# Optimization experiments

Measured on AMD Instinct MI355X. Metric: run time of the kernel, lower is better.

Reference implementation:

```python
import jax, jax.numpy as jnp
import numpy as np

EPS = 1e-5

def _conv3x3(x, w, b):
    # x: [B,C,H,W], w: [O,I,3,3], b: [O]; padding=1 preserves HxW
    y = jax.lax.conv_general_dilated(
        x, w, window_strides=(1, 1), padding=((1, 1), (1, 1)),
        dimension_numbers=('NCHW', 'OIHW', 'NCHW'))
    return y + b[None, :, None, None]

def _instance_norm(x):
    # InstanceNorm2d(affine=False): normalize over spatial dims per (sample, channel)
    mu = jnp.mean(x, axis=(2, 3), keepdims=True)
    var = jnp.var(x, axis=(2, 3), keepdims=True)
    return (x - mu) * jax.lax.rsqrt(var + EPS)

def setup_inputs() -> dict:
    key = jax.random.key(0)
    k1, k2, k3 = jax.random.split(key, 3)
    B, Cin, Cout, H, W = 8, 32, 64, 320, 320
    x = jax.random.normal(k1, (B, Cin, H, W), dtype=jnp.float32)
    w1 = jax.random.normal(k2, (Cout, Cin, 3, 3), dtype=jnp.float32) * (1.0 / np.sqrt(Cin * 9))
    b1 = jnp.zeros((Cout,), dtype=jnp.float32)
    w2 = jax.random.normal(k3, (Cout, Cout, 3, 3), dtype=jnp.float32) * (1.0 / np.sqrt(Cout * 9))
    b2 = jnp.zeros((Cout,), dtype=jnp.float32)
    return {"x": x, "w1": w1, "b1": b1, "w2": w2, "b2": b2}

def reference(x, w1, b1, w2, b2):
    # conv1 -> InstanceNorm -> ReLU -> (Dropout p=0 identity)
    h = jax.nn.relu(_instance_norm(_conv3x3(x, w1, b1)))
    # conv2 -> InstanceNorm -> ReLU -> (Dropout p=0 identity)
    out = jax.nn.relu(_instance_norm(_conv3x3(h, w2, b2)))
    return out
```

## Files before the change

kernel.cpp:

```cpp
#include <hip/hip_runtime.h>

#define HH 320
#define WW 320
#define BB 8
static constexpr float EPS = 1e-5f;

typedef __attribute__((ext_vector_type(8))) short bf16x8;
typedef __attribute__((ext_vector_type(4))) float f32x4;

__device__ inline float bf2f(unsigned short u) {
    union { unsigned int i; float f; } v; v.i = ((unsigned int)u) << 16; return v.f;
}
__device__ inline unsigned short f2bf(float f) {
    union { float f; unsigned int i; } v; v.f = f;
    unsigned int r = v.i + 0x7fffu + ((v.i >> 16) & 1u);
    return (unsigned short)(r >> 16);
}
__device__ inline unsigned int cvtpk(float a, float b) {
    unsigned int r;
    asm volatile("v_cvt_pk_bf16_f32 %0, %1, %2" : "=v"(r) : "v"(a), "v"(b));
    return r;
}
__device__ inline void glds16(const void* g, void* l) {
    __builtin_amdgcn_global_load_lds(
        (const __attribute__((address_space(1))) unsigned int*)g,
        (__attribute__((address_space(3))) unsigned int*)l, 16, 0, 0);
}

__global__ __launch_bounds__(256) void prep_hwc(const float* __restrict__ in,
                                                unsigned short* __restrict__ out)
{
    __shared__ float sT[32][65];
    const int tid = threadIdx.x;
    const int x0  = blockIdx.x * 64;
    const int y   = blockIdx.y;
    const int b   = blockIdx.z;
    for (int e = tid; e < 32 * 64; e += 256) {
        int c = e >> 6, x = e & 63;
        sT[c][x] = in[(((size_t)(b * 32 + c) * HH) + y) * WW + x0 + x];
    }
    __syncthreads();
    for (int e = tid; e < 64 * 32; e += 256) {
        int x = e >> 5, c = e & 31;
        out[((((size_t)b * HH + y) * WW) + x0 + x) * 32 + c] = f2bf(sT[c][x]);
    }
}

__global__ __launch_bounds__(256) void wprep_swz(const float* __restrict__ w1,
                                                 const float* __restrict__ w2,
                                                 unsigned short* __restrict__ wt1,
                                                 unsigned short* __restrict__ wt2)
{
    int i = blockIdx.x * 256 + threadIdx.x;
    if (i < 2304) {
        int s = i & 3, oc = (i >> 2) & 63, kk = i >> 8;
        int icq = s ^ ((oc >> 1) & 3);
        const float* src = w1 + ((size_t)oc * 32 + icq * 8) * 9 + kk;
        unsigned short pk[8];
#pragma unroll
        for (int j = 0; j < 8; ++j) pk[j] = f2bf(src[j * 9]);
        *(bf16x8*)&wt1[(size_t)i * 8] = *(bf16x8*)pk;
    }
    if (i < 4608) {
        int icc = i / 2304, u = i - icc * 2304;
        int s = u & 3, oc = (u >> 2) & 63, kk = u >> 8;
        int icq = s ^ ((oc >> 1) & 3);
        const float* src = w2 + ((size_t)oc * 64 + icc * 32 + icq * 8) * 9 + kk;
        unsigned short pk[8];
#pragma unroll
        for (int j = 0; j < 8; ++j) pk[j] = f2bf(src[j * 9]);
        *(bf16x8*)&wt2[(size_t)i * 8] = *(bf16x8*)pk;
    }
}

__global__ __launch_bounds__(256) void wfold(const unsigned short* __restrict__ wt2,
                                             const float* __restrict__ b2,
                                             const float2* __restrict__ stats1,
                                             unsigned short* __restrict__ wt2b,
                                             float* __restrict__ bias2b)
{
    __shared__ float sMu[64], sR[64];
    __shared__ float sBias[256];
    const int b = blockIdx.x, tid = threadIdx.x;
    if (tid < 64) {
        float2 ms = stats1[b * 64 + tid];
        sMu[tid] = bf2f(f2bf(ms.x));
        sR[tid]  = ms.y;
    }
    __syncthreads();
    const int oc = tid & 63, rep = tid >> 6;
    float bsum = 0.f;
    for (int cs = rep * 2; cs < rep * 2 + 2; ++cs) {
        int icc = cs >> 2, s = cs & 3;
        int icq = s ^ ((oc >> 1) & 3);
        for (int kk = 0; kk < 9; ++kk) {
            size_t u = (size_t)icc * 2304 + kk * 256 + oc * 4 + s;
            bf16x8 v = *(const bf16x8*)&wt2[u * 8];
            unsigned short o8[8];
#pragma unroll
            for (int j = 0; j < 8; ++j) {
                int ic = icc * 32 + icq * 8 + j;
                unsigned short wb = f2bf(bf2f(((unsigned short*)&v)[j]) * sR[ic]);
                o8[j] = wb;
                bsum += bf2f(wb) * sMu[ic];
            }
            *(bf16x8*)&wt2b[((size_t)b * 4608 + u) * 8] = *(bf16x8*)o8;
        }
    }
    sBias[tid] = bsum;
    __syncthreads();
    if (tid < 64) {
        float t = sBias[tid] + sBias[tid + 64] + sBias[tid + 128] + sBias[tid + 192];
        bias2b[b * 64 + tid] = b2[tid] - t;
    }
}

template<int CIN, int NORM>
__global__ __launch_bounds__(256, 2) void conv_mfma(
    const unsigned short* __restrict__ in_hwc,
    const float2* __restrict__ stats_in,
    const unsigned short* __restrict__ wt,
    const float* __restrict__ bias,
    unsigned short* __restrict__ out_hwc,
    float2* __restrict__ partials)
{
    constexpr int ICC = CIN / 32;
    constexpr int NG  = 4 * ICC;
    constexpr int NS  = NG * 3;

    __shared__ __align__(16) unsigned short sA[2][6 * 264 * 8];
    __shared__ __align__(16) unsigned short sWb[2][768 * 8];
    __shared__ float sRedS[256];
    __shared__ float sRedSS[256];
    __shared__ float sMaxMu[64];
    __shared__ unsigned short sMuBf[64];

    const int tid = threadIdx.x;
    const int x0  = blockIdx.x * 64;
    const int yb  = blockIdx.y * 16;
    const int b   = blockIdx.z;
    const int w   = tid >> 6;
    const int l   = tid & 63;
    const int lm  = l & 15;
    const int g   = l >> 4;

    const unsigned short* wtb = NORM ? wt + (size_t)b * 4608 * 8 : wt;
    const float* biasb        = NORM ? bias + b * 64 : bias;

    if (NORM) {
        if (tid < 64) {
            float2 ms = stats_in[b * 64 + tid];
            unsigned short mb = f2bf(ms.x);
            sMuBf[tid]  = mb;
            sMaxMu[tid] = bf2f(mb);
        }
        __syncthreads();
    }

    auto stage_slab = [&](int s2, int buf) {
        int kt2  = s2 % 3;
        int icc2 = (s2 / 3) % ICC;
        const unsigned short* wsrc = wtb + ((size_t)icc2 * 2304 + kt2 * 768) * 8;
        unsigned short* dst = &sWb[buf][0];
#pragma unroll
        for (int k = 0; k < 3; ++k)
            glds16(wsrc + (size_t)(k * 256 + w * 64 + l) * 8,
                   dst + (size_t)(k * 256 + w * 64) * 8);
    };

    auto issueA_glds = [&](int gi2) {
        int t2 = gi2 / ICC, icc2 = gi2 % ICC;
        int y02 = yb + t2 * 4;
        unsigned short* buf = &sA[gi2 & 1][0];
        for (int r = w; r < 6; r += 4) {
            int gy = y02 + r - 1;
            unsigned short* ldsrow = buf + r * 2112;
            if ((unsigned)gy < HH) {
                const unsigned short* rowbase =
                    in_hwc + ((size_t)(b * HH + gy) * WW) * CIN + icc2 * 32;
#pragma unroll
                for (int i = 0; i < 4; ++i) {
                    int u  = 4 + i * 64 + l;
                    int x  = u >> 2;
                    int cs = (u & 3) ^ ((x >> 1) & 3);
                    glds16(rowbase + (size_t)(x0 + x - 1) * CIN + cs * 8,
                           ldsrow + (size_t)(4 + i * 64) * 8);
                }
            } else {
                for (int u2 = l; u2 < 264; u2 += 64)
                    *(bf16x8*)(ldsrow + u2 * 8) = (bf16x8){0,0,0,0,0,0,0,0};
            }
        }
        if (tid < 48) {
            int icq = tid & 3, side = (tid >> 2) & 1, r = tid >> 3;
            int xs = side ? 65 : 0;
            int gy = y02 + r - 1, gx = x0 + xs - 1;
            bf16x8 v = (bf16x8){0,0,0,0,0,0,0,0};
            if ((unsigned)gy < HH && (unsigned)gx < WW)
                v = *(const bf16x8*)&in_hwc[(((size_t)(b * HH + gy) * WW) + gx) * CIN + icc2 * 32 + icq * 8];
            *(bf16x8*)&buf[(r * 264 + xs * 4 + icq) * 8] = v;
        }
    };

    bf16x8 ld[7];
    auto issueA_reg = [&](int gi2) {
        int t2 = gi2 / ICC, icc2 = gi2 % ICC;
        int y02 = yb + t2 * 4;
#pragma unroll
        for (int k = 0; k < 7; ++k) {
            int e = tid + k * 256;
            if (e < 1584) {
                int r = e / 264, rem = e - r * 264;
                int x = rem >> 2, icq = rem & 3;
                int gy = y02 + r - 1, gx = x0 + x - 1;
                if ((unsigned)gy < HH && (unsigned)gx < WW)
                    ld[k] = *(const bf16x8*)&in_hwc[(((size_t)(b * HH + gy) * WW) + gx) * CIN + icc2 * 32 + icq * 8];
            }
        }
    };
    auto writeA_reg = [&](int gi2) {
        int t2 = gi2 / ICC, icc2 = gi2 % ICC;
        int y02 = yb + t2 * 4;
        unsigned short* buf = &sA[gi2 & 1][0];
#pragma unroll
        for (int k = 0; k < 7; ++k) {
            int e = tid + k * 256;
            if (e < 1584) {
                int r = e / 264, rem = e - r * 264;
                int x = rem >> 2, icq = rem & 3;
                int gy = y02 + r - 1, gx = x0 + x - 1;
                int c0 = icc2 * 32 + icq * 8;
                unsigned int w4[4];
                if ((unsigned)gy < HH && (unsigned)gx < WW) {
#pragma unroll
                    for (int jp = 0; jp < 4; ++jp) {
                        float f0 = fmaxf(bf2f(((unsigned short*)&ld[k])[2 * jp]),     sMaxMu[c0 + 2 * jp]);
                        float f1 = fmaxf(bf2f(((unsigned short*)&ld[k])[2 * jp + 1]), sMaxMu[c0 + 2 * jp + 1]);
                        w4[jp] = cvtpk(f0, f1);
                    }
                } else {
#pragma unroll
                    for (int jp = 0; jp < 4; ++jp)
                        w4[jp] = (unsigned int)sMuBf[c0 + 2 * jp] |
                                 ((unsigned int)sMuBf[c0 + 2 * jp + 1] << 16);
                }
                *(uint4*)&buf[(r * 264 + x * 4 + (icq ^ ((x >> 1) & 3))) * 8] =
                    make_uint4(w4[0], w4[1], w4[2], w4[3]);
            }
        }
    };

    f32x4 acc[4][4];
#pragma unroll
    for (int fp = 0; fp < 4; ++fp)
#pragma unroll
        for (int fo = 0; fo < 4; ++fo)
            acc[fp][fo] = (f32x4){0.f, 0.f, 0.f, 0.f};

    float bb[4][4];
#pragma unroll
    for (int fo = 0; fo < 4; ++fo) {
        float4 b4 = *(const float4*)&biasb[fo * 16 + g * 4];
        bb[fo][0] = b4.x; bb[fo][1] = b4.y; bb[fo][2] = b4.z; bb[fo][3] = b4.w;
    }
    float sjA[4][4] = {}, qjA[4][4] = {};

    stage_slab(0, 0);
    if (NORM == 0) {
        issueA_glds(0);
    } else {
        issueA_reg(0);
        writeA_reg(0);
    }
    __syncthreads();

    for (int s = 0; s < NS; ++s) {
        const int kt = s % 3;
        const int gi = s / 3;
        const int icc = gi % ICC;
        const int t  = gi / ICC;

        if (s + 1 < NS) stage_slab(s + 1, (s + 1) & 1);
        if (kt == 0 && gi + 1 < NG) {
            if (NORM == 0) issueA_glds(gi + 1);
            else           issueA_reg(gi + 1);
        }

        {
            const unsigned short* bufA = &sA[gi & 1][0];
            const unsigned short* bufW = &sWb[s & 1][0];
            __builtin_amdgcn_s_setprio(1);
#pragma unroll
            for (int kx = 0; kx < 3; ++kx) {
                bf16x8 af[4], bfr[4];
#pragma unroll
                for (int fp = 0; fp < 4; ++fp) {
                    int xl = fp * 16 + lm + kx;
                    int u  = (xl * 4 + g) ^ ((xl >> 1) & 3);
                    af[fp] = *(const bf16x8*)(bufA + ((w + kt) * 264 + u) * 8);
                }
#pragma unroll
                for (int fo = 0; fo < 4; ++fo) {
                    int ocr = fo * 16 + lm;
                    int p   = (kx * 64 + ocr) * 4 + (g ^ ((ocr >> 1) & 3));
                    bfr[fo] = *(const bf16x8*)(bufW + p * 8);
                }
#pragma unroll
                for (int fo = 0; fo < 4; ++fo)
#pragma unroll
                    for (int fp = 0; fp < 4; ++fp)
                        acc[fp][fo] = __builtin_amdgcn_mfma_f32_16x16x32_bf16(
                            bfr[fo], af[fp], acc[fp][fo], 0, 0, 0);
            }
            __builtin_amdgcn_s_setprio(0);
        }

        if (kt == 2 && icc == ICC - 1) {
            const int row = yb + 4 * t + w;
#pragma unroll
            for (int fo = 0; fo < 4; ++fo) {
#pragma unroll
                for (int fp = 0; fp < 4; ++fp) {
                    float v0 = acc[fp][fo][0] + bb[fo][0], v1 = acc[fp][fo][1] + bb[fo][1];
                    float v2 = acc[fp][fo][2] + bb[fo][2], v3 = acc[fp][fo][3] + bb[fo][3];
                    sjA[fo][0] += v0; qjA[fo][0] += v0 * v0;
                    sjA[fo][1] += v1; qjA[fo][1] += v1 * v1;
                    sjA[fo][2] += v2; qjA[fo][2] += v2 * v2;
                    sjA[fo][3] += v3; qjA[fo][3] += v3 * v3;
                    uint2 st = make_uint2(cvtpk(v0, v1), cvtpk(v2, v3));
                    *(uint2*)&out_hwc[(((size_t)b * HH + row) * WW + x0 + fp * 16 + lm) * 64 + fo * 16 + g * 4] = st;
                    acc[fp][fo] = (f32x4){0.f, 0.f, 0.f, 0.f};
                }
            }
        }

        if (NORM == 1 && kt == 2 && gi + 1 < NG) writeA_reg(gi + 1);

        __syncthreads();
    }

#pragma unroll
    for (int fo = 0; fo < 4; ++fo) {
#pragma unroll
        for (int m = 1; m <= 8; m <<= 1)
#pragma unroll
            for (int j = 0; j < 4; ++j) {
                sjA[fo][j] += __shfl_xor(sjA[fo][j], m);
                qjA[fo][j] += __shfl_xor(qjA[fo][j], m);
            }
        if (lm == 0) {
#pragma unroll
            for (int j = 0; j < 4; ++j) {
                sRedS [w * 64 + fo * 16 + g * 4 + j] = sjA[fo][j];
                sRedSS[w * 64 + fo * 16 + g * 4 + j] = qjA[fo][j];
            }
        }
    }
    __syncthreads();
    if (tid < 64) {
        float S = 0.f, SS = 0.f;
#pragma unroll
        for (int q = 0; q < 4; ++q) { S += sRedS[q * 64 + tid]; SS += sRedSS[q * 64 + tid]; }
        partials[((size_t)b * 100 + blockIdx.y * 5 + blockIdx.x) * 64 + tid] = make_float2(S, SS);
    }
}

__global__ __launch_bounds__(256) void reduce_stats(const float2* __restrict__ partials,
                                                    float2* __restrict__ stats, int count)
{
    const int b  = blockIdx.x;
    const int oc = threadIdx.x & 63;
    const int q  = threadIdx.x >> 6;
    float s = 0.f, ss = 0.f;
    for (int i = q; i < count; i += 4) {
        float2 p = partials[((size_t)b * count + i) * 64 + oc];
        s += p.x; ss += p.y;
    }
    __shared__ float2 red[4][64];
    red[q][oc] = make_float2(s, ss);
    __syncthreads();
    if (threadIdx.x < 64) {
        float S = 0.f, SS = 0.f;
#pragma unroll
        for (int k = 0; k < 4; ++k) { S += red[k][threadIdx.x].x; SS += red[k][threadIdx.x].y; }
        const float n = (float)(HH * WW);
        float mean = S / n;
        float var  = fmaxf(SS / n - mean * mean, 0.f);
        stats[b * 64 + threadIdx.x] = make_float2(mean, rsqrtf(var + EPS));
    }
}

__global__ __launch_bounds__(256) void finalize_t(const unsigned short* __restrict__ h2,
                                                  const float2* __restrict__ stats,
                                                  float* __restrict__ out)
{
    __shared__ float2 sSt[64];
    const int tid = threadIdx.x;
    const int b   = blockIdx.z;
    if (tid < 64) sSt[tid] = stats[b * 64 + tid];
    __syncthreads();
    const int r   = tid >> 6;
    const int px  = tid & 63;
    const int row = blockIdx.y * 4 + r;
    const int x   = blockIdx.x * 64 + px;
    const unsigned short* src = h2 + ((size_t)(b * HH + row) * WW + x) * 64;
    bf16x8 v[8];
#pragma unroll
    for (int cq = 0; cq < 8; ++cq) v[cq] = *(const bf16x8*)(src + cq * 8);
#pragma unroll
    for (int cq = 0; cq < 8; ++cq)
#pragma unroll
        for (int j = 0; j < 8; ++j) {
            int c = cq * 8 + j;
            float2 ms = sSt[c];
            float f = fmaxf((bf2f(((unsigned short*)&v[cq])[j]) - ms.x) * ms.y, 0.f);
            out[((size_t)(b * 64 + c) * HH + row) * WW + x] = f;
        }
}

extern "C" void kernel_launch(void* const* d_in, const int* in_sizes, int n_in,
                              void* d_out, int out_size, void* d_ws, size_t ws_size,
                              hipStream_t stream)
{
    const float* x  = (const float*)d_in[0];
    const float* w1 = (const float*)d_in[1];
    const float* b1 = (const float*)d_in[2];
    const float* w2 = (const float*)d_in[3];
    const float* b2 = (const float*)d_in[4];
    float* out = (float*)d_out;

    char* ws = (char*)d_ws;
    unsigned short* h    = (unsigned short*)ws;
    float2* partials     = (float2*)(ws + 104857600);
    float2* stats1       = (float2*)(ws + 104857600 + 1638400);
    float2* stats2       = (float2*)(ws + 104857600 + 1638400 + 4096);
    unsigned short* reg2 = (unsigned short*)(ws + 104857600 + 1638400 + 8192);
    unsigned short* x_hwc = reg2;
    unsigned short* h2    = reg2;

    char* ob = (char*)d_out + 209715200;
    float*          bias2b = (float*)(ob - 2048);
    unsigned short* wt2b   = (unsigned short*)(ob - 2048 - 589824);
    unsigned short* wt2    = (unsigned short*)(ob - 2048 - 589824 - 73728);
    unsigned short* wt1    = (unsigned short*)(ob - 2048 - 589824 - 73728 - 36864);

    dim3 cgrid(5, 20, BB);

    wprep_swz<<<18, 256, 0, stream>>>(w1, w2, wt1, wt2);
    prep_hwc<<<dim3(5, HH, BB), 256, 0, stream>>>(x, x_hwc);

    conv_mfma<32, 0><<<cgrid, 256, 0, stream>>>(x_hwc, nullptr, wt1, b1, h, partials);
    reduce_stats<<<BB, 256, 0, stream>>>(partials, stats1, 100);
    wfold<<<BB, 256, 0, stream>>>(wt2, b2, stats1, wt2b, bias2b);
    conv_mfma<64, 1><<<cgrid, 256, 0, stream>>>(h, stats1, wt2b, bias2b, h2, partials);
    reduce_stats<<<BB, 256, 0, stream>>>(partials, stats2, 100);
    finalize_t<<<dim3(5, 80, BB), 256, 0, stream>>>(h2, stats2, out);
}
```

Before: 323.2 us.

## Read conv weights directly from global memory and split activation prefetch across taps

Removes the double-buffered LDS weight slab. Each MFMA tap now loads its weight fragments straight from global memory (an L2/L1-resident per-sample buffer), and the per-tap barrier loop is replaced by one barrier per input-channel group. The normalized-input path splits its register prefetch into two chunks interleaved with the tap computation, which lowers live register pressure, and the launch-bounds occupancy hint rises from 2 to 3 blocks. The trade-off is that every wave repeats the same global weight loads instead of sharing them through LDS, in exchange for fewer syncs and less LDS use.

New measurement: 749.6 us. 132% more time.

```diff
diff --git a/kernel.cpp b/kernel.cpp
--- a/kernel.cpp
+++ b/kernel.cpp
@@ -116,7 +116,7 @@
 }
 
 template<int CIN, int NORM>
-__global__ __launch_bounds__(256, 2) void conv_mfma(
+__global__ __launch_bounds__(256, 3) void conv_mfma(
     const unsigned short* __restrict__ in_hwc,
     const float2* __restrict__ stats_in,
     const unsigned short* __restrict__ wt,
@@ -126,10 +126,8 @@
 {
     constexpr int ICC = CIN / 32;
     constexpr int NG  = 4 * ICC;
-    constexpr int NS  = NG * 3;
 
     __shared__ __align__(16) unsigned short sA[2][6 * 264 * 8];
-    __shared__ __align__(16) unsigned short sWb[2][768 * 8];
     __shared__ float sRedS[256];
     __shared__ float sRedSS[256];
     __shared__ float sMaxMu[64];
@@ -154,19 +152,7 @@
             sMuBf[tid]  = mb;
             sMaxMu[tid] = bf2f(mb);
         }
-        __syncthreads();
-    }
-
-    auto stage_slab = [&](int s2, int buf) {
-        int kt2  = s2 % 3;
-        int icc2 = (s2 / 3) % ICC;
-        const unsigned short* wsrc = wtb + ((size_t)icc2 * 2304 + kt2 * 768) * 8;
-        unsigned short* dst = &sWb[buf][0];
-#pragma unroll
-        for (int k = 0; k < 3; ++k)
-            glds16(wsrc + (size_t)(k * 256 + w * 64 + l) * 8,
-                   dst + (size_t)(k * 256 + w * 64) * 8);
-    };
+    }
 
     auto issueA_glds = [&](int gi2) {
         int t2 = gi2 / ICC, icc2 = gi2 % ICC;
@@ -203,50 +189,44 @@
     };
 
     bf16x8 ld[7];
-    auto issueA_reg = [&](int gi2) {
+    auto issue_chunk = [&](int gi2, int k) {
         int t2 = gi2 / ICC, icc2 = gi2 % ICC;
         int y02 = yb + t2 * 4;
-#pragma unroll
-        for (int k = 0; k < 7; ++k) {
-            int e = tid + k * 256;
-            if (e < 1584) {
-                int r = e / 264, rem = e - r * 264;
-                int x = rem >> 2, icq = rem & 3;
-                int gy = y02 + r - 1, gx = x0 + x - 1;
-                if ((unsigned)gy < HH && (unsigned)gx < WW)
-                    ld[k] = *(const bf16x8*)&in_hwc[(((size_t)(b * HH + gy) * WW) + gx) * CIN + icc2 * 32 + icq * 8];
-            }
+        int e = tid + k * 256;
+        if (e < 1584) {
+            int r = e / 264, rem = e - r * 264;
+            int x = rem >> 2, icq = rem & 3;
+            int gy = y02 + r - 1, gx = x0 + x - 1;
+            if ((unsigned)gy < HH && (unsigned)gx < WW)
+                ld[k] = *(const bf16x8*)&in_hwc[(((size_t)(b * HH + gy) * WW) + gx) * CIN + icc2 * 32 + icq * 8];
         }
     };
-    auto writeA_reg = [&](int gi2) {
+    auto write_chunk = [&](int gi2, int k) {
         int t2 = gi2 / ICC, icc2 = gi2 % ICC;
         int y02 = yb + t2 * 4;
         unsigned short* buf = &sA[gi2 & 1][0];
-#pragma unroll
-        for (int k = 0; k < 7; ++k) {
-            int e = tid + k * 256;
-            if (e < 1584) {
-                int r = e / 264, rem = e - r * 264;
-                int x = rem >> 2, icq = rem & 3;
-                int gy = y02 + r - 1, gx = x0 + x - 1;
-                int c0 = icc2 * 32 + icq * 8;
-                unsigned int w4[4];
-                if ((unsigned)gy < HH && (unsigned)gx < WW) {
-#pragma unroll
-                    for (int jp = 0; jp < 4; ++jp) {
-                        float f0 = fmaxf(bf2f(((unsigned short*)&ld[k])[2 * jp]),     sMaxMu[c0 + 2 * jp]);
-                        float f1 = fmaxf(bf2f(((unsigned short*)&ld[k])[2 * jp + 1]), sMaxMu[c0 + 2 * jp + 1]);
-                        w4[jp] = cvtpk(f0, f1);
-                    }
-                } else {
-#pragma unroll
-                    for (int jp = 0; jp < 4; ++jp)
-                        w4[jp] = (unsigned int)sMuBf[c0 + 2 * jp] |
-                                 ((unsigned int)sMuBf[c0 + 2 * jp + 1] << 16);
+        int e = tid + k * 256;
+        if (e < 1584) {
+            int r = e / 264, rem = e - r * 264;
+            int x = rem >> 2, icq = rem & 3;
+            int gy = y02 + r - 1, gx = x0 + x - 1;
+            int c0 = icc2 * 32 + icq * 8;
+            unsigned int w4[4];
+            if ((unsigned)gy < HH && (unsigned)gx < WW) {
+#pragma unroll
+                for (int jp = 0; jp < 4; ++jp) {
+                    float f0 = fmaxf(bf2f(((unsigned short*)&ld[k])[2 * jp]),     sMaxMu[c0 + 2 * jp]);
+                    float f1 = fmaxf(bf2f(((unsigned short*)&ld[k])[2 * jp + 1]), sMaxMu[c0 + 2 * jp + 1]);
+                    w4[jp] = cvtpk(f0, f1);
                 }
-                *(uint4*)&buf[(r * 264 + x * 4 + (icq ^ ((x >> 1) & 3))) * 8] =
-                    make_uint4(w4[0], w4[1], w4[2], w4[3]);
-            }
+            } else {
+#pragma unroll
+                for (int jp = 0; jp < 4; ++jp)
+                    w4[jp] = (unsigned int)sMuBf[c0 + 2 * jp] |
+                             ((unsigned int)sMuBf[c0 + 2 * jp + 1] << 16);
+            }
+            *(uint4*)&buf[(r * 264 + x * 4 + (icq ^ ((x >> 1) & 3))) * 8] =
+                make_uint4(w4[0], w4[1], w4[2], w4[3]);
         }
     };
 
@@ -265,57 +245,79 @@
     }
     float sjA[4][4] = {}, qjA[4][4] = {};
 
-    stage_slab(0, 0);
+    auto tap = [&](int gi2, int kk) {
+        const int icc2 = gi2 % ICC;
+        const unsigned short* bufA = &sA[gi2 & 1][0];
+        const int ky = kk / 3, kx = kk - ky * 3;
+        bf16x8 af[4], bfr[4];
+#pragma unroll
+        for (int fp = 0; fp < 4; ++fp) {
+            int xl = fp * 16 + lm + kx;
+            int u  = (xl * 4 + g) ^ ((xl >> 1) & 3);
+            af[fp] = *(const bf16x8*)(bufA + ((w + ky) * 264 + u) * 8);
+        }
+#pragma unroll
+        for (int fo = 0; fo < 4; ++fo) {
+            int ocr = fo * 16 + lm;
+            size_t p = (size_t)icc2 * 2304 + kk * 256 + ocr * 4 + (g ^ ((ocr >> 1) & 3));
+            bfr[fo] = *(const bf16x8*)&wtb[p * 8];
+        }
+#pragma unroll
+        for (int fo = 0; fo < 4; ++fo)
+#pragma unroll
+            for (int fp = 0; fp < 4; ++fp)
+                acc[fp][fo] = __builtin_amdgcn_mfma_f32_16x16x32_bf16(
+                    bfr[fo], af[fp], acc[fp][fo], 0, 0, 0);
+    };
+
     if (NORM == 0) {
         issueA_glds(0);
+        __syncthreads();
     } else {
-        issueA_reg(0);
-        writeA_reg(0);
-    }
-    __syncthreads();
-
-    for (int s = 0; s < NS; ++s) {
-        const int kt = s % 3;
-        const int gi = s / 3;
-        const int icc = gi % ICC;
-        const int t  = gi / ICC;
-
-        if (s + 1 < NS) stage_slab(s + 1, (s + 1) & 1);
-        if (kt == 0 && gi + 1 < NG) {
-            if (NORM == 0) issueA_glds(gi + 1);
-            else           issueA_reg(gi + 1);
-        }
-
-        {
-            const unsigned short* bufA = &sA[gi & 1][0];
-            const unsigned short* bufW = &sWb[s & 1][0];
+#pragma unroll
+        for (int k = 0; k < 7; ++k) issue_chunk(0, k);
+        __syncthreads();
+#pragma unroll
+        for (int k = 0; k < 7; ++k) write_chunk(0, k);
+        __syncthreads();
+    }
+
+    for (int gi = 0; gi < NG; ++gi) {
+        const int icc = gi % ICC, t = gi / ICC;
+        const bool more = (gi + 1 < NG);
+
+        if (NORM == 0) {
+            if (more) issueA_glds(gi + 1);
             __builtin_amdgcn_s_setprio(1);
 #pragma unroll
-            for (int kx = 0; kx < 3; ++kx) {
-                bf16x8 af[4], bfr[4];
-#pragma unroll
-                for (int fp = 0; fp < 4; ++fp) {
-                    int xl = fp * 16 + lm + kx;
-                    int u  = (xl * 4 + g) ^ ((xl >> 1) & 3);
-                    af[fp] = *(const bf16x8*)(bufA + ((w + kt) * 264 + u) * 8);
-                }
-#pragma unroll
-                for (int fo = 0; fo < 4; ++fo) {
-                    int ocr = fo * 16 + lm;
-                    int p   = (kx * 64 + ocr) * 4 + (g ^ ((ocr >> 1) & 3));
-                    bfr[fo] = *(const bf16x8*)(bufW + p * 8);
-                }
-#pragma unroll
-                for (int fo = 0; fo < 4; ++fo)
-#pragma unroll
-                    for (int fp = 0; fp < 4; ++fp)
-                        acc[fp][fo] = __builtin_amdgcn_mfma_f32_16x16x32_bf16(
-                            bfr[fo], af[fp], acc[fp][fo], 0, 0, 0);
-            }
+            for (int kk = 0; kk < 9; ++kk) tap(gi, kk);
             __builtin_amdgcn_s_setprio(0);
-        }
-
-        if (kt == 2 && icc == ICC - 1) {
+        } else {
+            if (more) {
+#pragma unroll
+                for (int k = 0; k < 4; ++k) issue_chunk(gi + 1, k);
+            }
+            __builtin_amdgcn_s_setprio(1);
+#pragma unroll
+            for (int kk = 0; kk < 4; ++kk) tap(gi, kk);
+            __builtin_amdgcn_s_setprio(0);
+            if (more) {
+#pragma unroll
+                for (int k = 0; k < 4; ++k) write_chunk(gi + 1, k);
+#pragma unroll
+                for (int k = 4; k < 7; ++k) issue_chunk(gi + 1, k);
+            }
+            __builtin_amdgcn_s_setprio(1);
+#pragma unroll
+            for (int kk = 4; kk < 9; ++kk) tap(gi, kk);
+            __builtin_amdgcn_s_setprio(0);
+            if (more) {
+#pragma unroll
+                for (int k = 4; k < 7; ++k) write_chunk(gi + 1, k);
+            }
+        }
+
+        if (icc == ICC - 1) {
             const int row = yb + 4 * t + w;
 #pragma unroll
             for (int fo = 0; fo < 4; ++fo) {
@@ -333,9 +335,6 @@
                 }
             }
         }
-
-        if (NORM == 1 && kt == 2 && gi + 1 < NG) writeA_reg(gi + 1);
-
         __syncthreads();
     }
 
```

## Pad activations with guard borders and hand-pipeline conv stages with fine-grained waits

Applied to the files above, without the earlier changes.

Input and intermediate activations are stored in padded 322x322 layouts: a zero border for x and a -inf (0xFF80) guard border for h, so that max with mu yields the mu fold value. This removes the per-element boundary checks in the conv kernels. The two conv kernels are split into specialized versions, and the per-slab __syncthreads loop is replaced by explicit vmcnt waits, raw s_barrier and sched_barrier to overlap weight and activation loads with MFMA work. The scheme relies on exact vmcnt counts and adds a small guard-init kernel, so a wrong count risks races.

New measurement: 426.9 us. +32.1%, slower.

```diff
diff --git a/kernel.cpp b/kernel.cpp
--- a/kernel.cpp
+++ b/kernel.cpp
@@ -2,11 +2,17 @@
 
 #define HH 320
 #define WW 320
+#define PW 322
 #define BB 8
 static constexpr float EPS = 1e-5f;
 
 typedef __attribute__((ext_vector_type(8))) short bf16x8;
 typedef __attribute__((ext_vector_type(4))) float f32x4;
+
+#define VMW(N) asm volatile("s_waitcnt vmcnt(" #N ")" ::: "memory")
+#define LGKM0  asm volatile("s_waitcnt lgkmcnt(0)" ::: "memory")
+#define SBAR() __builtin_amdgcn_s_barrier()
+#define SCH0() __builtin_amdgcn_sched_barrier(0)
 
 __device__ inline float bf2f(unsigned short u) {
     union { unsigned int i; float f; } v; v.i = ((unsigned int)u) << 16; return v.f;
@@ -27,23 +33,50 @@
         (__attribute__((address_space(3))) unsigned int*)l, 16, 0, 0);
 }
 
-__global__ __launch_bounds__(256) void prep_hwc(const float* __restrict__ in,
-                                                unsigned short* __restrict__ out)
+__global__ __launch_bounds__(256) void prep_pad(const float* __restrict__ in,
+                                                unsigned short* __restrict__ xp)
 {
     __shared__ float sT[32][65];
     const int tid = threadIdx.x;
-    const int x0  = blockIdx.x * 64;
-    const int y   = blockIdx.y;
+    const int p0  = blockIdx.x * 64;
+    const int py  = blockIdx.y;
     const int b   = blockIdx.z;
+    const int gy  = py - 1;
+    unsigned short* orow = xp + ((size_t)(b * PW + py) * PW) * 32;
+    if ((unsigned)gy >= (unsigned)HH) {
+        for (int e = tid; e < 64 * 32; e += 256) {
+            int x = e >> 5, c = e & 31;
+            int p = p0 + x;
+            if (p < PW) orow[(size_t)p * 32 + c] = 0;
+        }
+        return;
+    }
     for (int e = tid; e < 32 * 64; e += 256) {
-        int c = e >> 6, x = e & 63;
-        sT[c][x] = in[(((size_t)(b * 32 + c) * HH) + y) * WW + x0 + x];
+        int c = e >> 6, i = e & 63;
+        int gx = p0 + i - 1;
+        sT[c][i] = ((unsigned)gx < (unsigned)WW)
+                   ? in[(((size_t)(b * 32 + c) * HH) + gy) * WW + gx] : 0.f;
     }
     __syncthreads();
     for (int e = tid; e < 64 * 32; e += 256) {
         int x = e >> 5, c = e & 31;
-        out[((((size_t)b * HH + y) * WW) + x0 + x) * 32 + c] = f2bf(sT[c][x]);
-    }
+        int p = p0 + x;
+        if (p < PW) orow[(size_t)p * 32 + c] = f2bf(sT[c][x]);
+    }
+}
+
+__global__ __launch_bounds__(256) void init_guards(unsigned short* __restrict__ hp)
+{
+    int i = blockIdx.x * 256 + threadIdx.x;
+    if (i >= BB * 1284) return;
+    int b = i / 1284, p = i - b * 1284;
+    int row, col;
+    if (p < 322)      { row = 0;   col = p; }
+    else if (p < 644) { row = 321; col = p - 322; }
+    else { int q = p - 644; row = 1 + (q >> 1); col = (q & 1) ? 321 : 0; }
+    unsigned short* d = hp + ((size_t)(b * PW + row) * PW + col) * 64;
+#pragma unroll
+    for (int k = 0; k < 64; ++k) d[k] = 0xFF80;
 }
 
 __global__ __launch_bounds__(256) void wprep_swz(const float* __restrict__ w1,
@@ -115,230 +148,331 @@
     }
 }
 
-template<int CIN, int NORM>
-__global__ __launch_bounds__(256, 2) void conv_mfma(
-    const unsigned short* __restrict__ in_hwc,
+__global__ __launch_bounds__(256, 2) void conv1_pipe(
+    const unsigned short* __restrict__ xp,
+    const unsigned short* __restrict__ wt,
+    const float* __restrict__ bias,
+    unsigned short* __restrict__ hp,
+    float2* __restrict__ partials)
+{
+    __shared__ __align__(16) unsigned short sA[2][1584 * 8];
+    __shared__ __align__(16) unsigned short sW[2][768 * 8];
+    __shared__ float sRedS[256], sRedSS[256];
+
+    const int tid = threadIdx.x;
+    const int XB  = blockIdx.x * 64;
+    const int yb  = blockIdx.y * 16;
+    const int b   = blockIdx.z;
+    const int w = tid >> 6, l = tid & 63, lm = l & 15, g = l >> 4;
+
+    auto issueA = [&](int gg, int bufi) {
+        const int y0 = yb + gg * 4;
+        unsigned short* buf = sA[bufi];
+#pragma unroll
+        for (int j = 0; j < 3; ++j) {
+            const int hrow = 3 * w + j;
+            const int r = hrow >> 1, half = hrow & 1;
+            const unsigned short* rowb = xp + ((size_t)(b * PW + y0 + r) * PW + XB) * 32;
+            unsigned short* dst = buf + (r * 264 + half * 132) * 8;
+#pragma unroll
+            for (int i = 0; i < 2; ++i) {
+                int xu = half * 132 + i * 64 + l;
+                int x = xu >> 2, cs = (xu & 3) ^ ((x >> 1) & 3);
+                glds16(rowb + (size_t)x * 32 + cs * 8, dst + (size_t)(i * 64) * 8);
+            }
+            if (l < 4) {
+                int xu = half * 132 + 128 + l;
+                int x = xu >> 2, cs = (xu & 3) ^ ((x >> 1) & 3);
+                glds16(rowb + (size_t)x * 32 + cs * 8, dst + (size_t)128 * 8);
+            }
+        }
+    };
+    auto issueW = [&](int kt, int bufi) {
+        const unsigned short* wsrc = wt + (size_t)(kt * 768) * 8;
+        unsigned short* dst = sW[bufi];
+#pragma unroll
+        for (int k = 0; k < 3; ++k)
+            glds16(wsrc + (size_t)(k * 256 + w * 64 + l) * 8,
+                   dst + (size_t)(k * 256 + w * 64) * 8);
+    };
+
+    f32x4 acc[4][4];
+#pragma unroll
+    for (int fp = 0; fp < 4; ++fp)
+#pragma unroll
+        for (int fo = 0; fo < 4; ++fo) acc[fp][fo] = (f32x4){0.f,0.f,0.f,0.f};
+
+    float bb[4][4];
+#pragma unroll
+    for (int fo = 0; fo < 4; ++fo) {
+        float4 b4 = *(const float4*)&bias[fo * 16 + g * 4];
+        bb[fo][0] = b4.x; bb[fo][1] = b4.y; bb[fo][2] = b4.z; bb[fo][3] = b4.w;
+    }
+    float sjA[4][4] = {}, qjA[4][4] = {};
+
+    auto compute = [&](int bufA, int bufW, int kt) {
+        const unsigned short* A  = sA[bufA];
+        const unsigned short* Wb = sW[bufW];
+        __builtin_amdgcn_s_setprio(1);
+#pragma unroll
+        for (int kx = 0; kx < 3; ++kx) {
+            bf16x8 af[4], bfr[4];
+#pragma unroll
+            for (int fp = 0; fp < 4; ++fp) {
+                int xl = fp * 16 + lm + kx;
+                int u  = (xl * 4 + g) ^ ((xl >> 1) & 3);
+                af[fp] = *(const bf16x8*)(A + ((w + kt) * 264 + u) * 8);
+            }
+#pragma unroll
+            for (int fo = 0; fo < 4; ++fo) {
+                int ocr = fo * 16 + lm;
+                bfr[fo] = *(const bf16x8*)(Wb + (kx * 256 + ocr * 4 + (g ^ ((ocr >> 1) & 3))) * 8);
+            }
+#pragma unroll
+            for (int fo = 0; fo < 4; ++fo)
+#pragma unroll
+                for (int fp = 0; fp < 4; ++fp)
+                    acc[fp][fo] = __builtin_amdgcn_mfma_f32_16x16x32_bf16(
+                        bfr[fo], af[fp], acc[fp][fo], 0, 0, 0);
+        }
+        __builtin_amdgcn_s_setprio(0);
+    };
+
+    auto epilogue = [&](int t) {
+        const int prow = yb + 4 * t + w + 1;
+#pragma unroll
+        for (int fo = 0; fo < 4; ++fo) {
+#pragma unroll
+            for (int fp = 0; fp < 4; ++fp) {
+                float v0 = acc[fp][fo][0] + bb[fo][0], v1 = acc[fp][fo][1] + bb[fo][1];
+                float v2 = acc[fp][fo][2] + bb[fo][2], v3 = acc[fp][fo][3] + bb[fo][3];
+                sjA[fo][0] += v0; qjA[fo][0] += v0 * v0;
+                sjA[fo][1] += v1; qjA[fo][1] += v1 * v1;
+                sjA[fo][2] += v2; qjA[fo][2] += v2 * v2;
+                sjA[fo][3] += v3; qjA[fo][3] += v3 * v3;
+                uint2 st = make_uint2(cvtpk(v0, v1), cvtpk(v2, v3));
+                *(uint2*)&hp[((size_t)(b * PW + prow) * PW + XB + 1 + fp * 16 + lm) * 64 + fo * 16 + g * 4] = st;
+                acc[fp][fo] = (f32x4){0.f,0.f,0.f,0.f};
+            }
+        }
+    };
+
+    issueW(0, 0);
+    issueA(0, 0);
+    __syncthreads();
+
+    for (int gi = 0; gi < 4; ++gi) {
+        const int ba = gi & 1;
+        issueW(1, ba ^ 1);
+        VMW(19); SBAR(); SCH0();
+        compute(ba, ba, 0);
+        SBAR(); SCH0();
+        issueW(2, ba);
+        VMW(3); SBAR(); SCH0();
+        compute(ba, ba ^ 1, 1);
+        SBAR(); SCH0();
+        issueW(0, ba ^ 1);
+        issueA((gi < 3) ? gi + 1 : 3, ba ^ 1);
+        VMW(12); SBAR(); SCH0();
+        compute(ba, ba, 2);
+        epilogue(gi);
+        SBAR(); SCH0();
+    }
+    __syncthreads();
+
+#pragma unroll
+    for (int fo = 0; fo < 4; ++fo) {
+#pragma unroll
+        for (int m = 1; m <= 8; m <<= 1)
+#pragma unroll
+            for (int j = 0; j < 4; ++j) {
+                sjA[fo][j] += __shfl_xor(sjA[fo][j], m);
+                qjA[fo][j] += __shfl_xor(qjA[fo][j], m);
+            }
+        if (lm == 0) {
+#pragma unroll
+            for (int j = 0; j < 4; ++j) {
+                sRedS [w * 64 + fo * 16 + g * 4 + j] = sjA[fo][j];
+                sRedSS[w * 64 + fo * 16 + g * 4 + j] = qjA[fo][j];
+            }
+        }
+    }
+    __syncthreads();
+    if (tid < 64) {
+        float S = 0.f, SS = 0.f;
+#pragma unroll
+        for (int q = 0; q < 4; ++q) { S += sRedS[q * 64 + tid]; SS += sRedSS[q * 64 + tid]; }
+        partials[((size_t)b * 100 + blockIdx.y * 5 + blockIdx.x) * 64 + tid] = make_float2(S, SS);
+    }
+}
+
+__global__ __launch_bounds__(256, 2) void conv2_pipe(
+    const unsigned short* __restrict__ hpin,
     const float2* __restrict__ stats_in,
     const unsigned short* __restrict__ wt,
     const float* __restrict__ bias,
-    unsigned short* __restrict__ out_hwc,
+    unsigned short* __restrict__ h2,
     float2* __restrict__ partials)
 {
-    constexpr int ICC = CIN / 32;
-    constexpr int NG  = 4 * ICC;
-    constexpr int NS  = NG * 3;
-
-    __shared__ __align__(16) unsigned short sA[2][6 * 264 * 8];
-    __shared__ __align__(16) unsigned short sWb[2][768 * 8];
-    __shared__ float sRedS[256];
-    __shared__ float sRedSS[256];
+    __shared__ __align__(16) unsigned short sA[2][1584 * 8];
+    __shared__ __align__(16) unsigned short sW[2][768 * 8];
+    __shared__ float sRedS[256], sRedSS[256];
     __shared__ float sMaxMu[64];
-    __shared__ unsigned short sMuBf[64];
 
     const int tid = threadIdx.x;
-    const int x0  = blockIdx.x * 64;
+    const int XB  = blockIdx.x * 64;
     const int yb  = blockIdx.y * 16;
     const int b   = blockIdx.z;
-    const int w   = tid >> 6;
-    const int l   = tid & 63;
-    const int lm  = l & 15;
-    const int g   = l >> 4;
-
-    const unsigned short* wtb = NORM ? wt + (size_t)b * 4608 * 8 : wt;
-    const float* biasb        = NORM ? bias + b * 64 : bias;
-
-    if (NORM) {
-        if (tid < 64) {
-            float2 ms = stats_in[b * 64 + tid];
-            unsigned short mb = f2bf(ms.x);
-            sMuBf[tid]  = mb;
-            sMaxMu[tid] = bf2f(mb);
-        }
-        __syncthreads();
-    }
-
-    auto stage_slab = [&](int s2, int buf) {
-        int kt2  = s2 % 3;
-        int icc2 = (s2 / 3) % ICC;
-        const unsigned short* wsrc = wtb + ((size_t)icc2 * 2304 + kt2 * 768) * 8;
-        unsigned short* dst = &sWb[buf][0];
+    const int w = tid >> 6, l = tid & 63, lm = l & 15, g = l >> 4;
+
+    const unsigned short* wtb = wt + (size_t)b * 4608 * 8;
+
+    if (tid < 64) {
+        float2 ms = stats_in[b * 64 + tid];
+        sMaxMu[tid] = bf2f(f2bf(ms.x));
+    }
+
+    bf16x8 ld[7];
+    auto issueR = [&](int gg) {
+        const int t2 = gg >> 1, icc2 = gg & 1;
+        const int y0 = yb + t2 * 4;
+#pragma unroll
+        for (int k = 0; k < 7; ++k) {
+            int e = w * 396 + k * 64 + l;
+            if (k < 6 || l < 12) {
+                int r = e / 264, xu = e - r * 264;
+                int x = xu >> 2, icq = xu & 3;
+                ld[k] = *(const bf16x8*)&hpin[((size_t)(b * PW + y0 + r) * PW + XB + x) * 64 + icc2 * 32 + icq * 8];
+            }
+        }
+    };
+    auto writeA = [&](int gg) {
+        unsigned short* buf = sA[gg & 1];
+        const int c0b = (gg & 1) * 32;
+#pragma unroll
+        for (int k = 0; k < 7; ++k) {
+            int e = w * 396 + k * 64 + l;
+            if (k < 6 || l < 12) {
+                int r = e / 264, xu = e - r * 264;
+                int x = xu >> 2, icq = xu & 3;
+                int c0 = c0b + icq * 8;
+                unsigned int w4[4];
+#pragma unroll
+                for (int jp = 0; jp < 4; ++jp) {
+                    float f0 = fmaxf(bf2f(((unsigned short*)&ld[k])[2 * jp]),     sMaxMu[c0 + 2 * jp]);
+                    float f1 = fmaxf(bf2f(((unsigned short*)&ld[k])[2 * jp + 1]), sMaxMu[c0 + 2 * jp + 1]);
+                    w4[jp] = cvtpk(f0, f1);
+                }
+                *(uint4*)&buf[(r * 264 + x * 4 + (icq ^ ((x >> 1) & 3))) * 8] =
+                    make_uint4(w4[0], w4[1], w4[2], w4[3]);
+            }
+        }
+    };
+    auto issueW = [&](int icc2, int kt, int bufi) {
+        const unsigned short* wsrc = wtb + (size_t)(icc2 * 2304 + kt * 768) * 8;
+        unsigned short* dst = sW[bufi];
 #pragma unroll
         for (int k = 0; k < 3; ++k)
             glds16(wsrc + (size_t)(k * 256 + w * 64 + l) * 8,
                    dst + (size_t)(k * 256 + w * 64) * 8);
     };
 
-    auto issueA_glds = [&](int gi2) {
-        int t2 = gi2 / ICC, icc2 = gi2 % ICC;
-        int y02 = yb + t2 * 4;
-        unsigned short* buf = &sA[gi2 & 1][0];
-        for (int r = w; r < 6; r += 4) {
-            int gy = y02 + r - 1;
-            unsigned short* ldsrow = buf + r * 2112;
-            if ((unsigned)gy < HH) {
-                const unsigned short* rowbase =
-                    in_hwc + ((size_t)(b * HH + gy) * WW) * CIN + icc2 * 32;
-#pragma unroll
-                for (int i = 0; i < 4; ++i) {
-                    int u  = 4 + i * 64 + l;
-                    int x  = u >> 2;
-                    int cs = (u & 3) ^ ((x >> 1) & 3);
-                    glds16(rowbase + (size_t)(x0 + x - 1) * CIN + cs * 8,
-                           ldsrow + (size_t)(4 + i * 64) * 8);
-                }
-            } else {
-                for (int u2 = l; u2 < 264; u2 += 64)
-                    *(bf16x8*)(ldsrow + u2 * 8) = (bf16x8){0,0,0,0,0,0,0,0};
-            }
-        }
-        if (tid < 48) {
-            int icq = tid & 3, side = (tid >> 2) & 1, r = tid >> 3;
-            int xs = side ? 65 : 0;
-            int gy = y02 + r - 1, gx = x0 + xs - 1;
-            bf16x8 v = (bf16x8){0,0,0,0,0,0,0,0};
-            if ((unsigned)gy < HH && (unsigned)gx < WW)
-                v = *(const bf16x8*)&in_hwc[(((size_t)(b * HH + gy) * WW) + gx) * CIN + icc2 * 32 + icq * 8];
-            *(bf16x8*)&buf[(r * 264 + xs * 4 + icq) * 8] = v;
-        }
-    };
-
-    bf16x8 ld[7];
-    auto issueA_reg = [&](int gi2) {
-        int t2 = gi2 / ICC, icc2 = gi2 % ICC;
-        int y02 = yb + t2 * 4;
-#pragma unroll
-        for (int k = 0; k < 7; ++k) {
-            int e = tid + k * 256;
-            if (e < 1584) {
-                int r = e / 264, rem = e - r * 264;
-                int x = rem >> 2, icq = rem & 3;
-                int gy = y02 + r - 1, gx = x0 + x - 1;
-                if ((unsigned)gy < HH && (unsigned)gx < WW)
-                    ld[k] = *(const bf16x8*)&in_hwc[(((size_t)(b * HH + gy) * WW) + gx) * CIN + icc2 * 32 + icq * 8];
-            }
-        }
-    };
-    auto writeA_reg = [&](int gi2) {
-        int t2 = gi2 / ICC, icc2 = gi2 % ICC;
-        int y02 = yb + t2 * 4;
-        unsigned short* buf = &sA[gi2 & 1][0];
-#pragma unroll
-        for (int k = 0; k < 7; ++k) {
-            int e = tid + k * 256;
-            if (e < 1584) {
-                int r = e / 264, rem = e - r * 264;
-                int x = rem >> 2, icq = rem & 3;
-                int gy = y02 + r - 1, gx = x0 + x - 1;
-                int c0 = icc2 * 32 + icq * 8;
-                unsigned int w4[4];
-                if ((unsigned)gy < HH && (unsigned)gx < WW) {
-#pragma unroll
-                    for (int jp = 0; jp < 4; ++jp) {
-                        float f0 = fmaxf(bf2f(((unsigned short*)&ld[k])[2 * jp]),     sMaxMu[c0 + 2 * jp]);
-                        float f1 = fmaxf(bf2f(((unsigned short*)&ld[k])[2 * jp + 1]), sMaxMu[c0 + 2 * jp + 1]);
-                        w4[jp] = cvtpk(f0, f1);
-                    }
-                } else {
-#pragma unroll
-                    for (int jp = 0; jp < 4; ++jp)
-                        w4[jp] = (unsigned int)sMuBf[c0 + 2 * jp] |
-                                 ((unsigned int)sMuBf[c0 + 2 * jp + 1] << 16);
-                }
-                *(uint4*)&buf[(r * 264 + x * 4 + (icq ^ ((x >> 1) & 3))) * 8] =
-                    make_uint4(w4[0], w4[1], w4[2], w4[3]);
-            }
-        }
-    };
-
     f32x4 acc[4][4];
 #pragma unroll
     for (int fp = 0; fp < 4; ++fp)
 #pragma unroll
-        for (int fo = 0; fo < 4; ++fo)
-            acc[fp][fo] = (f32x4){0.f, 0.f, 0.f, 0.f};
+        for (int fo = 0; fo < 4; ++fo) acc[fp][fo] = (f32x4){0.f,0.f,0.f,0.f};
 
     float bb[4][4];
 #pragma unroll
     for (int fo = 0; fo < 4; ++fo) {
-        float4 b4 = *(const float4*)&biasb[fo * 16 + g * 4];
+        float4 b4 = *(const float4*)&bias[b * 64 + fo * 16 + g * 4];
         bb[fo][0] = b4.x; bb[fo][1] = b4.y; bb[fo][2] = b4.z; bb[fo][3] = b4.w;
     }
     float sjA[4][4] = {}, qjA[4][4] = {};
 
-    stage_slab(0, 0);
-    if (NORM == 0) {
-        issueA_glds(0);
-    } else {
-        issueA_reg(0);
-        writeA_reg(0);
-    }
-    __syncthreads();
-
-    for (int s = 0; s < NS; ++s) {
-        const int kt = s % 3;
-        const int gi = s / 3;
-        const int icc = gi % ICC;
-        const int t  = gi / ICC;
-
-        if (s + 1 < NS) stage_slab(s + 1, (s + 1) & 1);
-        if (kt == 0 && gi + 1 < NG) {
-            if (NORM == 0) issueA_glds(gi + 1);
-            else           issueA_reg(gi + 1);
-        }
-
-        {
-            const unsigned short* bufA = &sA[gi & 1][0];
-            const unsigned short* bufW = &sWb[s & 1][0];
-            __builtin_amdgcn_s_setprio(1);
-#pragma unroll
-            for (int kx = 0; kx < 3; ++kx) {
-                bf16x8 af[4], bfr[4];
-#pragma unroll
-                for (int fp = 0; fp < 4; ++fp) {
-                    int xl = fp * 16 + lm + kx;
-                    int u  = (xl * 4 + g) ^ ((xl >> 1) & 3);
-                    af[fp] = *(const bf16x8*)(bufA + ((w + kt) * 264 + u) * 8);
-                }
-#pragma unroll
-                for (int fo = 0; fo < 4; ++fo) {
-                    int ocr = fo * 16 + lm;
-                    int p   = (kx * 64 + ocr) * 4 + (g ^ ((ocr >> 1) & 3));
-                    bfr[fo] = *(const bf16x8*)(bufW + p * 8);
-                }
-#pragma unroll
-                for (int fo = 0; fo < 4; ++fo)
-#pragma unroll
-                    for (int fp = 0; fp < 4; ++fp)
-                        acc[fp][fo] = __builtin_amdgcn_mfma_f32_16x16x32_bf16(
-                            bfr[fo], af[fp], acc[fp][fo], 0, 0, 0);
-            }
-            __builtin_amdgcn_s_setprio(0);
-        }
-
-        if (kt == 2 && icc == ICC - 1) {
-            const int row = yb + 4 * t + w;
+    auto compute = [&](int bufA, int bufW, int kt) {
+        const unsigned short* A  = sA[bufA];
+        const unsigned short* Wb = sW[bufW];
+        __builtin_amdgcn_s_setprio(1);
+#pragma unroll
+        for (int kx = 0; kx < 3; ++kx) {
+            bf16x8 af[4], bfr[4];
+#pragma unroll
+            for (int fp = 0; fp < 4; ++fp) {
+                int xl = fp * 16 + lm + kx;
+                int u  = (xl * 4 + g) ^ ((xl >> 1) & 3);
+                af[fp] = *(const bf16x8*)(A + ((w + kt) * 264 + u) * 8);
+            }
 #pragma unroll
             for (int fo = 0; fo < 4; ++fo) {
-#pragma unroll
-                for (int fp = 0; fp < 4; ++fp) {
-                    float v0 = acc[fp][fo][0] + bb[fo][0], v1 = acc[fp][fo][1] + bb[fo][1];
-                    float v2 = acc[fp][fo][2] + bb[fo][2], v3 = acc[fp][fo][3] + bb[fo][3];
-                    sjA[fo][0] += v0; qjA[fo][0] += v0 * v0;
-                    sjA[fo][1] += v1; qjA[fo][1] += v1 * v1;
-                    sjA[fo][2] += v2; qjA[fo][2] += v2 * v2;
-                    sjA[fo][3] += v3; qjA[fo][3] += v3 * v3;
-                    uint2 st = make_uint2(cvtpk(v0, v1), cvtpk(v2, v3));
-                    *(uint2*)&out_hwc[(((size_t)b * HH + row) * WW + x0 + fp * 16 + lm) * 64 + fo * 16 + g * 4] = st;
-                    acc[fp][fo] = (f32x4){0.f, 0.f, 0.f, 0.f};
-                }
-            }
-        }
-
-        if (NORM == 1 && kt == 2 && gi + 1 < NG) writeA_reg(gi + 1);
-
-        __syncthreads();
-    }
-
+                int ocr = fo * 16 + lm;
+                bfr[fo] = *(const bf16x8*)(Wb + (kx * 256 + ocr * 4 + (g ^ ((ocr >> 1) & 3))) * 8);
+            }
+#pragma unroll
+            for (int fo = 0; fo < 4; ++fo)
+#pragma unroll
+                for (int fp = 0; fp < 4; ++fp)
+                    acc[fp][fo] = __builtin_amdgcn_mfma_f32_16x16x32_bf16(
+                        bfr[fo], af[fp], acc[fp][fo], 0, 0, 0);
+        }
+        __builtin_amdgcn_s_setprio(0);
+    };
+
+    auto epilogue = [&](int t) {
+        const int row = yb + 4 * t + w;
+#pragma unroll
+        for (int fo = 0; fo < 4; ++fo) {
+#pragma unroll
+            for (int fp = 0; fp < 4; ++fp) {
+                float v0 = acc[fp][fo][0] + bb[fo][0], v1 = acc[fp][fo][1] + bb[fo][1];
+                float v2 = acc[fp][fo][2] + bb[fo][2], v3 = acc[fp][fo][3] + bb[fo][3];
+                sjA[fo][0] += v0; qjA[fo][0] += v0 * v0;
+                sjA[fo][1] += v1; qjA[fo][1] += v1 * v1;
+                sjA[fo][2] += v2; qjA[fo][2] += v2 * v2;
+                sjA[fo][3] += v3; qjA[fo][3] += v3 * v3;
+                uint2 st = make_uint2(cvtpk(v0, v1), cvtpk(v2, v3));
+                *(uint2*)&h2[(((size_t)b * HH + row) * WW + XB + fp * 16 + lm) * 64 + fo * 16 + g * 4] = st;
+                acc[fp][fo] = (f32x4){0.f,0.f,0.f,0.f};
+            }
+        }
+    };
+
+    issueW(0, 0, 0);
+    issueR(0);
+    __syncthreads();
+    writeA(0);
+    __syncthreads();
+
+#define C2GROUP(GI, VMP0)                                                   \
+    {                                                                       \
+        const int gi_ = (GI);                                               \
+        const int ba_ = gi_ & 1;                                            \
+        issueR((gi_ < 7) ? gi_ + 1 : 7);                                    \
+        issueW(ba_, 1, ba_ ^ 1);                                            \
+        VMW(VMP0); SBAR(); SCH0();                                          \
+        compute(ba_, ba_, 0);                                               \
+        SBAR(); SCH0();                                                     \
+        issueW(ba_, 2, ba_);                                                \
+        VMW(3); SBAR(); SCH0();                                             \
+        compute(ba_, ba_ ^ 1, 1);                                           \
+        SBAR(); SCH0();                                                     \
+        issueW(ba_ ^ 1, 0, ba_ ^ 1);                                        \
+        VMW(3); SBAR(); SCH0();                                             \
+        compute(ba_, ba_, 2);                                               \
+        if (ba_ == 1) epilogue(gi_ >> 1);                                   \
+        if (gi_ < 7) writeA(gi_ + 1);                                       \
+        LGKM0;                                                              \
+        SBAR(); SCH0();                                                     \
+    }
+
+    for (int gp = 0; gp < 4; ++gp) {
+        C2GROUP(gp * 2,     26);
+        C2GROUP(gp * 2 + 1, 10);
+    }
+#undef C2GROUP
+
+    __syncthreads();
 #pragma unroll
     for (int fo = 0; fo < 4; ++fo) {
 #pragma unroll
@@ -430,29 +564,30 @@
     float* out = (float*)d_out;
 
     char* ws = (char*)d_ws;
-    unsigned short* h    = (unsigned short*)ws;
-    float2* partials     = (float2*)(ws + 104857600);
-    float2* stats1       = (float2*)(ws + 104857600 + 1638400);
-    float2* stats2       = (float2*)(ws + 104857600 + 1638400 + 4096);
-    unsigned short* reg2 = (unsigned short*)(ws + 104857600 + 1638400 + 8192);
-    unsigned short* x_hwc = reg2;
-    unsigned short* h2    = reg2;
+    unsigned short* hp   = (unsigned short*)ws;
+    unsigned short* reg2 = (unsigned short*)(ws + 106172416);
+    unsigned short* xp   = reg2;
+    unsigned short* h2   = reg2;
+    float2* stats1 = (float2*)(ws + 106172416 + 104857600);
+    float2* stats2 = stats1 + 512;
 
     char* ob = (char*)d_out + 209715200;
-    float*          bias2b = (float*)(ob - 2048);
-    unsigned short* wt2b   = (unsigned short*)(ob - 2048 - 589824);
-    unsigned short* wt2    = (unsigned short*)(ob - 2048 - 589824 - 73728);
-    unsigned short* wt1    = (unsigned short*)(ob - 2048 - 589824 - 73728 - 36864);
+    float2*         partials = (float2*)(ob - 409600);
+    float*          bias2b   = (float*)(ob - 409600 - 2048);
+    unsigned short* wt2b     = (unsigned short*)(ob - 409600 - 2048 - 589824);
+    unsigned short* wt2      = (unsigned short*)(ob - 409600 - 2048 - 589824 - 73728);
+    unsigned short* wt1      = (unsigned short*)(ob - 409600 - 2048 - 589824 - 73728 - 36864);
 
     dim3 cgrid(5, 20, BB);
 
     wprep_swz<<<18, 256, 0, stream>>>(w1, w2, wt1, wt2);
-    prep_hwc<<<dim3(5, HH, BB), 256, 0, stream>>>(x, x_hwc);
-
-    conv_mfma<32, 0><<<cgrid, 256, 0, stream>>>(x_hwc, nullptr, wt1, b1, h, partials);
+    init_guards<<<(BB * 1284 + 255) / 256, 256, 0, stream>>>(hp);
+    prep_pad<<<dim3(6, PW, BB), 256, 0, stream>>>(x, xp);
+
+    conv1_pipe<<<cgrid, 256, 0, stream>>>(xp, wt1, b1, hp, partials);
     reduce_stats<<<BB, 256, 0, stream>>>(partials, stats1, 100);
     wfold<<<BB, 256, 0, stream>>>(wt2, b2, stats1, wt2b, bias2b);
-    conv_mfma<64, 1><<<cgrid, 256, 0, stream>>>(h, stats1, wt2b, bias2b, h2, partials);
+    conv2_pipe<<<cgrid, 256, 0, stream>>>(hp, stats1, wt2b, bias2b, h2, partials);
     reduce_stats<<<BB, 256, 0, stream>>>(partials, stats2, 100);
     finalize_t<<<dim3(5, 80, BB), 256, 0, stream>>>(h2, stats2, out);
 }
```
